# Kernel tuning notes

Measured on AMD Instinct MI355X. Metric: run time of the kernel, lower is better.

The kernel has to match this reference:

```python
import jax, jax.numpy as jnp
import numpy as np

# Instant-NGP hash grid constants (match init_kwargs)
N_MAX, N_MIN = 2048.0, 16.0
L, T, F, DIM = 16, 2**19, 2, 3
NV = 2**DIM  # 8 corners of a voxel
# primes stored as int32 in the original (2654435761 wraps negative) -> replicate exactly
PIS = jnp.asarray(np.array([1, 2654435761, 805459861], dtype=np.uint32).astype(np.int32))
# bin_mask[v, d] = True -> corner v takes floor along dim d
_neigs = np.arange(NV, dtype=np.int64)[:, None]
_dims = np.arange(DIM, dtype=np.int64)[None, :]
BIN_MASK = jnp.asarray((_neigs & (1 << _dims)) == 0)  # [8, 3]
# per-level grid resolutions N_l = N_min * b**l
_b = np.exp((np.log(N_MAX) - np.log(N_MIN)) / L)
SCALES = jnp.asarray((N_MIN * _b ** np.arange(L)).astype(np.float32))  # [L]


def setup_inputs() -> dict:
    key = jax.random.key(0)
    k1, k2 = jax.random.split(key)
    N = 2_000_000
    x = jax.random.uniform(k1, (N, DIM), dtype=jnp.float32)  # points in [0,1)^3 (mu=0, sigma=1)
    # per-level embedding tables, init U(-1e-4, 1e-4) as in the torch module
    W = jax.random.uniform(k2, (L, T, F), minval=-1e-4, maxval=1e-4, dtype=jnp.float32)
    return {"x": x, "W": W}


def _hash(idxs):
    # idxs: [N, 8, 3] int32. int32 wraparound multiply matches low 32 bits of the
    # torch int64 product; since T is a power of two and Python-style mod of a
    # negative by a positive only depends on the low log2(T) bits, result matches.
    prod = idxs * PIS  # [N, 8, 3] int32 (wraps)
    h = prod[..., 0] ^ prod[..., 1] ^ prod[..., 2]
    return h % T  # jnp remainder follows sign of divisor -> nonnegative


def _encode(x, W):
    def level(carry, level_args):
        scale, Wl = level_args
        un_x = x * scale                                   # [N, 3]
        x0 = un_x.astype(jnp.int32)                        # trunc == floor for x >= 0
        diff = jax.lax.stop_gradient(un_x - x0.astype(un_x.dtype))  # [N, 3], detached as in torch
        # corner integer coords: floor where bin_mask else floor+1
        idxs = jnp.where(BIN_MASK[None], x0[:, None, :], x0[:, None, :] + 1)  # [N, 8, 3]
        fv = Wl[_hash(idxs)]                               # [N, 8, F] gather
        wts = jnp.where(BIN_MASK[None], 1.0 - diff[:, None, :], diff[:, None, :])
        wts = wts.prod(axis=-1, keepdims=True)             # [N, 8, 1] trilinear weights
        return carry, (fv * wts).sum(axis=-2)              # [N, F]

    _, ys = jax.lax.scan(level, 0, (SCALES, W))            # [L, N, F]
    # original writes level l into y[:, l*F:(l+1)*F]
    return jnp.transpose(ys, (1, 0, 2)).reshape(x.shape[0], L * F)


def reference(x, W):
    return _encode(x, W)
```

## Files before the change

kernel.cpp:

```cpp
#include <hip/hip_runtime.h>
#include <hip/hip_fp16.h>
#include <math.h>

#define NLEV 16
#define TBLN (1u << 19)
#define TMASK (TBLN - 1u)
#define NPT 4
#define NPTL 16
#define NPTL2 8
#define PR1 2654435761u
#define PR2 805459861u

typedef float f32x4 __attribute__((ext_vector_type(4)));
typedef unsigned int u32;
typedef unsigned int u32x2 __attribute__((ext_vector_type(2)));
typedef unsigned int u32x4 __attribute__((ext_vector_type(4)));

struct ScaleArgs { float s[NLEV]; };

#define DU0 18
#define DU1 23
#define DU2 31
#define GU0 0
#define GU1 5832
#define GU2 17999
#define GUTOT 47790
#define DD2 31
#define DD5 75
#define PO2 0
#define PO5 28830
#define GPTOT2 445080
#define DD3 41
#define DD4 55
#define QO3 0
#define QO4 65600
#define GQTOT 225980

static __device__ __forceinline__ u32 packf2(float a, float b) {
    __half2 h = __floats2half2_rn(a, b);
    return __builtin_bit_cast(u32, h);
}
static __device__ __forceinline__ float2 unpack16(u32 u) {
    __half2 h = __builtin_bit_cast(__half2, u);
    return __half22float2(h);
}
static __device__ __forceinline__ u32 sel4(u32x4 P, u32 idx) {
    u32 s0 = (idx & 1u) ? P.y : P.x;
    u32 s1 = (idx & 1u) ? P.w : P.z;
    return (idx & 2u) ? s1 : s0;
}

__global__ __launch_bounds__(256)
void convert_w(const float* __restrict__ W, u32* __restrict__ Wh, int np4)
{
    int i = blockIdx.x * blockDim.x + threadIdx.x;
    if (i >= np4) return;
    const f32x4* src = reinterpret_cast<const f32x4*>(W) + (size_t)i * 2;
    f32x4 A = __builtin_nontemporal_load(src);
    f32x4 B = __builtin_nontemporal_load(src + 1);
    u32x4 o = { packf2(A.x, A.y), packf2(A.z, A.w),
                packf2(B.x, B.y), packf2(B.z, B.w) };
    __builtin_nontemporal_store(o, reinterpret_cast<u32x4*>(Wh) + i);
}

__global__ __launch_bounds__(256)
void build_unpaired(const float* __restrict__ Wlf, u32* __restrict__ Gu, int D, int P)
{
    int v = blockIdx.x * blockDim.x + threadIdx.x;
    if (v >= P) return;
    int ix = v % D;
    int rest = v / D;
    int iy = rest % D;
    int iz = rest / D;
    u32 h = (((u32)iy * PR1) ^ ((u32)iz * PR2) ^ (u32)ix) & TMASK;
    float2 f = *reinterpret_cast<const float2*>(Wlf + (size_t)h * 2u);
    Gu[v] = packf2(f.x, f.y);
}

__global__ __launch_bounds__(256)
void build_dense(const float* __restrict__ Wlf, u32x2* __restrict__ Gpl, int D, int P)
{
    int v = blockIdx.x * blockDim.x + threadIdx.x;
    if (v >= P) return;
    int Dx = D - 1;
    int ix = v % Dx;
    int rest = v / Dx;
    int iy = rest % D;
    int iz = rest / D;
    u32 e = ((u32)iy * PR1) ^ ((u32)iz * PR2);
    u32 h0 = (e ^ (u32)ix) & TMASK;
    u32 h1 = (e ^ (u32)(ix + 1)) & TMASK;
    float2 f0 = *reinterpret_cast<const float2*>(Wlf + (size_t)h0 * 2u);
    float2 f1 = *reinterpret_cast<const float2*>(Wlf + (size_t)h1 * 2u);
    u32x2 o = { packf2(f0.x, f0.y), packf2(f1.x, f1.y) };
    Gpl[v] = o;
}

__global__ __launch_bounds__(256)
void build_dense16(const float* __restrict__ Wlf, u32x4* __restrict__ Gql, int D, int P)
{
    int v = blockIdx.x * blockDim.x + threadIdx.x;
    if (v >= P) return;
    int Dx = D - 1;
    int ix = v % Dx;
    int rest = v / Dx;
    int iy = rest % Dx;
    int iz = rest / Dx;
    u32 ey0 = ((u32)iy * PR1) ^ ((u32)iz * PR2);
    u32 ey1 = ((u32)(iy + 1) * PR1) ^ ((u32)iz * PR2);
    u32 h00 = (ey0 ^ (u32)ix) & TMASK;
    u32 h10 = (ey0 ^ (u32)(ix + 1)) & TMASK;
    u32 h01 = (ey1 ^ (u32)ix) & TMASK;
    u32 h11 = (ey1 ^ (u32)(ix + 1)) & TMASK;
    float2 f00 = *reinterpret_cast<const float2*>(Wlf + (size_t)h00 * 2u);
    float2 f10 = *reinterpret_cast<const float2*>(Wlf + (size_t)h10 * 2u);
    float2 f01 = *reinterpret_cast<const float2*>(Wlf + (size_t)h01 * 2u);
    float2 f11 = *reinterpret_cast<const float2*>(Wlf + (size_t)h11 * 2u);
    u32x4 o = { packf2(f00.x, f00.y), packf2(f10.x, f10.y),
                packf2(f01.x, f01.y), packf2(f11.x, f11.y) };
    Gql[v] = o;
}

template<int D>
static __device__ __forceinline__ u32 lds_interp(const u32* g, float ux, float uy, float uz)
{
    int ix = (int)ux, iy = (int)uy, iz = (int)uz;
    float dx = ux - (float)ix, dy = uy - (float)iy, dz = uz - (float)iz;
    int b = (iz * D + iy) * D + ix;
    u32 c0 = g[b],             c1 = g[b + 1];
    u32 c2 = g[b + D],         c3 = g[b + D + 1];
    u32 c4 = g[b + D * D],     c5 = g[b + D * D + 1];
    u32 c6 = g[b + D * D + D], c7 = g[b + D * D + D + 1];
    float wxl = 1.f - dx, wxh = dx;
    float wyl = 1.f - dy, wyh = dy;
    float wzl = 1.f - dz, wzh = dz;
    float ax = 0.f, ay = 0.f;
    float2 f;
    f = unpack16(c0); { float w = (wxl * wyl) * wzl; ax = fmaf(f.x, w, ax); ay = fmaf(f.y, w, ay); }
    f = unpack16(c1); { float w = (wxh * wyl) * wzl; ax = fmaf(f.x, w, ax); ay = fmaf(f.y, w, ay); }
    f = unpack16(c2); { float w = (wxl * wyh) * wzl; ax = fmaf(f.x, w, ax); ay = fmaf(f.y, w, ay); }
    f = unpack16(c3); { float w = (wxh * wyh) * wzl; ax = fmaf(f.x, w, ax); ay = fmaf(f.y, w, ay); }
    f = unpack16(c4); { float w = (wxl * wyl) * wzh; ax = fmaf(f.x, w, ax); ay = fmaf(f.y, w, ay); }
    f = unpack16(c5); { float w = (wxh * wyl) * wzh; ax = fmaf(f.x, w, ax); ay = fmaf(f.y, w, ay); }
    f = unpack16(c6); { float w = (wxl * wyh) * wzh; ax = fmaf(f.x, w, ax); ay = fmaf(f.y, w, ay); }
    f = unpack16(c7); { float w = (wxh * wyh) * wzh; ax = fmaf(f.x, w, ax); ay = fmaf(f.y, w, ay); }
    return packf2(ax, ay);
}

template<int D>
__global__ __launch_bounds__(256)
void lds_level(const float* __restrict__ x, const u32* __restrict__ Gu,
               u32* __restrict__ scl, float scale, int N)
{
    __shared__ u32 g[D * D * D];
    for (int i = threadIdx.x; i < D * D * D; i += 256) g[i] = Gu[i];
    __syncthreads();

    int base = blockIdx.x * (256 * NPTL);
    #pragma unroll 4
    for (int i = 0; i < NPTL; ++i) {
        int n = base + i * 256 + (int)threadIdx.x;
        if (n < N) {
            float px = __builtin_nontemporal_load(&x[(size_t)n * 3 + 0]);
            float py = __builtin_nontemporal_load(&x[(size_t)n * 3 + 1]);
            float pz = __builtin_nontemporal_load(&x[(size_t)n * 3 + 2]);
            __builtin_nontemporal_store(
                lds_interp<D>(g, px * scale, py * scale, pz * scale), scl + n);
        }
    }
}

template<int D>
__global__ __launch_bounds__(512)
void lds_level_dyn(const float* __restrict__ x, const u32* __restrict__ Gu,
                   u32* __restrict__ scl, float scale, int N)
{
    extern __shared__ u32 g[];
    for (int i = threadIdx.x; i < D * D * D; i += 512) g[i] = Gu[i];
    __syncthreads();

    int base = blockIdx.x * (512 * NPTL2);
    #pragma unroll 4
    for (int i = 0; i < NPTL2; ++i) {
        int n = base + i * 512 + (int)threadIdx.x;
        if (n < N) {
            float px = __builtin_nontemporal_load(&x[(size_t)n * 3 + 0]);
            float py = __builtin_nontemporal_load(&x[(size_t)n * 3 + 1]);
            float pz = __builtin_nontemporal_load(&x[(size_t)n * 3 + 2]);
            __builtin_nontemporal_store(
                lds_interp<D>(g, px * scale, py * scale, pz * scale), scl + n);
        }
    }
}


template<int D>
static __device__ __forceinline__ void dense_body(
    const float* __restrict__ x, const u32x2* __restrict__ Gp,
    u32* __restrict__ scl, float scale, int N, int TOT, int t)
{
    constexpr int Dx = D - 1;
    constexpr int zstep = D * Dx;

    int nn[NPT];
    float dx[NPT], dy[NPT], dz[NPT];
    int base[NPT];
    u32x2 P0[NPT], P1[NPT], P2[NPT], P3[NPT];

    #pragma unroll
    for (int i = 0; i < NPT; ++i) {
        int n = t + i * TOT;
        if (n > N - 1) n = N - 1;
        nn[i] = n;
        float px = __builtin_nontemporal_load(&x[(size_t)n * 3 + 0]);
        float py = __builtin_nontemporal_load(&x[(size_t)n * 3 + 1]);
        float pz = __builtin_nontemporal_load(&x[(size_t)n * 3 + 2]);
        float ux = px * scale, uy = py * scale, uz = pz * scale;
        int ix = (int)ux, iy = (int)uy, iz = (int)uz;
        dx[i] = ux - (float)ix;
        dy[i] = uy - (float)iy;
        dz[i] = uz - (float)iz;
        base[i] = (iz * D + iy) * Dx + ix;
    }

    #pragma unroll
    for (int i = 0; i < NPT; ++i) {
        int b = base[i];
        P0[i] = Gp[b];
        P1[i] = Gp[b + Dx];
        P2[i] = Gp[b + zstep];
        P3[i] = Gp[b + zstep + Dx];
    }

    #pragma unroll
    for (int i = 0; i < NPT; ++i) {
        float ax = 0.f, ay = 0.f;
        float wxl = 1.f - dx[i], wxh = dx[i];
        float wyl = 1.f - dy[i], wyh = dy[i];
        float wzl = 1.f - dz[i], wzh = dz[i];
        {
            float2 f0 = unpack16(P0[i].x), f1 = unpack16(P0[i].y);
            float w0 = (wxl * wyl) * wzl, w1 = (wxh * wyl) * wzl;
            ax = fmaf(f0.x, w0, ax); ay = fmaf(f0.y, w0, ay);
            ax = fmaf(f1.x, w1, ax); ay = fmaf(f1.y, w1, ay);
        }
        {
            float2 f0 = unpack16(P1[i].x), f1 = unpack16(P1[i].y);
            float w0 = (wxl * wyh) * wzl, w1 = (wxh * wyh) * wzl;
            ax = fmaf(f0.x, w0, ax); ay = fmaf(f0.y, w0, ay);
            ax = fmaf(f1.x, w1, ax); ay = fmaf(f1.y, w1, ay);
        }
        {
            float2 f0 = unpack16(P2[i].x), f1 = unpack16(P2[i].y);
            float w0 = (wxl * wyl) * wzh, w1 = (wxh * wyl) * wzh;
            ax = fmaf(f0.x, w0, ax); ay = fmaf(f0.y, w0, ay);
            ax = fmaf(f1.x, w1, ax); ay = fmaf(f1.y, w1, ay);
        }
        {
            float2 f0 = unpack16(P3[i].x), f1 = unpack16(P3[i].y);
            float w0 = (wxl * wyh) * wzh, w1 = (wxh * wyh) * wzh;
            ax = fmaf(f0.x, w0, ax); ay = fmaf(f0.y, w0, ay);
            ax = fmaf(f1.x, w1, ax); ay = fmaf(f1.y, w1, ay);
        }
        __builtin_nontemporal_store(packf2(ax, ay), scl + nn[i]);
    }
}

template<int D>
static __device__ __forceinline__ void dense16_body(
    const float* __restrict__ x, const u32x4* __restrict__ Gq,
    u32* __restrict__ scl, float scale, int N, int TOT, int t)
{
    constexpr int Dx = D - 1;
    constexpr int zstep = Dx * Dx;

    int nn[NPT];
    float dx[NPT], dy[NPT], dz[NPT];
    int base[NPT];
    u32x4 Q0[NPT], Q1[NPT];

    #pragma unroll
    for (int i = 0; i < NPT; ++i) {
        int n = t + i * TOT;
        if (n > N - 1) n = N - 1;
        nn[i] = n;
        float px = __builtin_nontemporal_load(&x[(size_t)n * 3 + 0]);
        float py = __builtin_nontemporal_load(&x[(size_t)n * 3 + 1]);
        float pz = __builtin_nontemporal_load(&x[(size_t)n * 3 + 2]);
        float ux = px * scale, uy = py * scale, uz = pz * scale;
        int ix = (int)ux, iy = (int)uy, iz = (int)uz;
        dx[i] = ux - (float)ix;
        dy[i] = uy - (float)iy;
        dz[i] = uz - (float)iz;
        base[i] = (iz * Dx + iy) * Dx + ix;
    }

    #pragma unroll
    for (int i = 0; i < NPT; ++i) {
        Q0[i] = Gq[base[i]];
        Q1[i] = Gq[base[i] + zstep];
    }

    #pragma unroll
    for (int i = 0; i < NPT; ++i) {
        float ax = 0.f, ay = 0.f;
        float wxl = 1.f - dx[i], wxh = dx[i];
        float wyl = 1.f - dy[i], wyh = dy[i];
        float wzl = 1.f - dz[i], wzh = dz[i];
        float2 f;
        f = unpack16(Q0[i].x); { float w = (wxl * wyl) * wzl; ax = fmaf(f.x, w, ax); ay = fmaf(f.y, w, ay); }
        f = unpack16(Q0[i].y); { float w = (wxh * wyl) * wzl; ax = fmaf(f.x, w, ax); ay = fmaf(f.y, w, ay); }
        f = unpack16(Q0[i].z); { float w = (wxl * wyh) * wzl; ax = fmaf(f.x, w, ax); ay = fmaf(f.y, w, ay); }
        f = unpack16(Q0[i].w); { float w = (wxh * wyh) * wzl; ax = fmaf(f.x, w, ax); ay = fmaf(f.y, w, ay); }
        f = unpack16(Q1[i].x); { float w = (wxl * wyl) * wzh; ax = fmaf(f.x, w, ax); ay = fmaf(f.y, w, ay); }
        f = unpack16(Q1[i].y); { float w = (wxh * wyl) * wzh; ax = fmaf(f.x, w, ax); ay = fmaf(f.y, w, ay); }
        f = unpack16(Q1[i].z); { float w = (wxl * wyh) * wzh; ax = fmaf(f.x, w, ax); ay = fmaf(f.y, w, ay); }
        f = unpack16(Q1[i].w); { float w = (wxh * wyh) * wzh; ax = fmaf(f.x, w, ax); ay = fmaf(f.y, w, ay); }
        __builtin_nontemporal_store(packf2(ax, ay), scl + nn[i]);
    }
}

static __device__ __forceinline__ void hash_body(
    const float* __restrict__ x, const u32* __restrict__ Wl,
    u32* __restrict__ scl, float scale, int N, int TOT, int t)
{
    int nn[NPT];
    float dx[NPT], dy[NPT], dz[NPT];
    u32 a0[NPT], a1[NPT], a2[NPT];
    u32 fv[NPT][8];

    #pragma unroll
    for (int i = 0; i < NPT; ++i) {
        int n = t + i * TOT;
        if (n > N - 1) n = N - 1;
        nn[i] = n;
        float px = __builtin_nontemporal_load(&x[(size_t)n * 3 + 0]);
        float py = __builtin_nontemporal_load(&x[(size_t)n * 3 + 1]);
        float pz = __builtin_nontemporal_load(&x[(size_t)n * 3 + 2]);
        float ux = px * scale, uy = py * scale, uz = pz * scale;
        int ix = (int)ux, iy = (int)uy, iz = (int)uz;
        dx[i] = ux - (float)ix;
        dy[i] = uy - (float)iy;
        dz[i] = uz - (float)iz;
        a0[i] = (unsigned)ix;
        a1[i] = (unsigned)iy * PR1;
        a2[i] = (unsigned)iz * PR2;
    }

    #pragma unroll
    for (int i = 0; i < NPT; ++i) {
        u32 b0 = a0[i] + 1u, b1 = a1[i] + PR1, b2 = a2[i] + PR2;
        u32 E[4] = { a1[i] ^ a2[i], b1 ^ a2[i], a1[i] ^ b2, b1 ^ b2 };
        u32 par = a0[i] & 3u;
        if ((par & 1u) == 0u) {
            #pragma unroll
            for (int j = 0; j < 4; ++j) {
                u32 hl = (E[j] ^ a0[i]) & TMASK;
                u32x2 p = *reinterpret_cast<const u32x2*>(Wl + (hl & ~1u));
                fv[i][2 * j + 0] = (hl & 1u) ? p.y : p.x;
                fv[i][2 * j + 1] = (hl & 1u) ? p.x : p.y;
            }
        } else if (par == 1u) {
            #pragma unroll
            for (int j = 0; j < 4; ++j) {
                u32 hl = (E[j] ^ a0[i]) & TMASK;
                u32x4 P = *reinterpret_cast<const u32x4*>(Wl + (hl & ~3u));
                u32 il = hl & 3u;
                fv[i][2 * j + 0] = sel4(P, il);
                fv[i][2 * j + 1] = sel4(P, il ^ 3u);
            }
        } else {
            #pragma unroll
            for (int j = 0; j < 4; ++j) {
                u32 hl = (E[j] ^ a0[i]) & TMASK;
                u32 hh = (E[j] ^ b0) & TMASK;
                fv[i][2 * j + 0] = Wl[hl];
                fv[i][2 * j + 1] = Wl[hh];
            }
        }
    }

    #pragma unroll
    for (int i = 0; i < NPT; ++i) {
        float ax = 0.f, ay = 0.f;
        #pragma unroll
        for (int v = 0; v < 8; ++v) {
            float wx = (v & 1) ? dx[i] : 1.f - dx[i];
            float wy = (v & 2) ? dy[i] : 1.f - dy[i];
            float wz = (v & 4) ? dz[i] : 1.f - dz[i];
            float w = (wx * wy) * wz;
            float2 f = unpack16(fv[i][v]);
            ax = fmaf(f.x, w, ax);
            ay = fmaf(f.y, w, ay);
        }
        __builtin_nontemporal_store(packf2(ax, ay), scl + nn[i]);
    }
}

__global__ __launch_bounds__(256)
void fused_levels(const float* __restrict__ x, const u32* __restrict__ Wh,
                  const u32x2* __restrict__ Gp, const u32x4* __restrict__ Gq,
                  u32* __restrict__ scratch,
                  ScaleArgs sc, int N, int TOT, int BPL, int lstart)
{
    int li = blockIdx.x / BPL;
    int lvl = li + lstart;
    int t = (blockIdx.x - li * BPL) * blockDim.x + threadIdx.x;
    if (t >= TOT) return;
    float scale = sc.s[lvl];
    u32* scl = scratch + (size_t)lvl * (size_t)N;

    switch (lvl) {
        case 2: dense_body<DD2>(x, Gp + PO2, scl, scale, N, TOT, t); break;
        case 3: dense16_body<DD3>(x, Gq + QO3, scl, scale, N, TOT, t); break;
        case 4: dense16_body<DD4>(x, Gq + QO4, scl, scale, N, TOT, t); break;
        case 5: dense_body<DD5>(x, Gp + PO5, scl, scale, N, TOT, t); break;
        default:
            hash_body(x, Wh + (size_t)(lvl - 6) * TBLN, scl, scale, N, TOT, t);
            break;
    }
}

__global__ __launch_bounds__(256)
void transpose_kernel(const u32* __restrict__ sc, float* __restrict__ out, int N)
{
    __shared__ u32 lds[16][257];
    int P0 = blockIdx.x * 256;
    int t = threadIdx.x;
    #pragma unroll
    for (int l = 0; l < NLEV; ++l) {
        int n = P0 + t;
        if (n < N) lds[l][t] = __builtin_nontemporal_load(sc + (size_t)l * N + n);
    }
    __syncthreads();
    int w = t >> 6, l6 = t & 63;
    #pragma unroll
    for (int k = 0; k < 8; ++k) {
        int p = w * 64 + k * 8 + (l6 >> 3);
        int c = l6 & 7;
        if (P0 + p < N) {
            float2 f0 = unpack16(lds[2 * c][p]);
            float2 f1 = unpack16(lds[2 * c + 1][p]);
            f32x4 v = { f0.x, f0.y, f1.x, f1.y };
            __builtin_nontemporal_store(v,
                reinterpret_cast<f32x4*>(out + (size_t)(P0 + p) * 32u + (size_t)c * 4u));
        }
    }
}

__global__ __launch_bounds__(256)
void hashenc_fallback(const float* __restrict__ x, const float* __restrict__ W,
                      float* __restrict__ out, ScaleArgs sc, int N)
{
    int n = blockIdx.x * blockDim.x + threadIdx.x;
    if (n >= N) return;
    float px = x[(size_t)n * 3 + 0];
    float py = x[(size_t)n * 3 + 1];
    float pz = x[(size_t)n * 3 + 2];
    float acc[2 * NLEV];
    #pragma unroll
    for (int l = 0; l < NLEV; ++l) {
        float s = sc.s[l];
        float ux = px * s, uy = py * s, uz = pz * s;
        int ix = (int)ux, iy = (int)uy, iz = (int)uz;
        float dx = ux - (float)ix, dy = uy - (float)iy, dz = uz - (float)iz;
        unsigned a0 = (unsigned)ix;
        unsigned a1 = (unsigned)iy * PR1;
        unsigned a2 = (unsigned)iz * PR2;
        unsigned b0 = a0 + 1u, b1 = a1 + PR1, b2 = a2 + PR2;
        const float* Wl = W + (size_t)l * TBLN * 2u;
        float ax = 0.f, ay = 0.f;
        #pragma unroll
        for (int v = 0; v < 8; ++v) {
            unsigned h = ((v & 1) ? b0 : a0) ^ ((v & 2) ? b1 : a1) ^ ((v & 4) ? b2 : a2);
            h &= TMASK;
            float wx = (v & 1) ? dx : 1.f - dx;
            float wy = (v & 2) ? dy : 1.f - dy;
            float wz = (v & 4) ? dz : 1.f - dz;
            float w = (wx * wy) * wz;
            const float2 fvv = *reinterpret_cast<const float2*>(Wl + (size_t)h * 2u);
            ax = fmaf(fvv.x, w, ax);
            ay = fmaf(fvv.y, w, ay);
        }
        acc[2 * l + 0] = ax;
        acc[2 * l + 1] = ay;
    }
    float4* o = reinterpret_cast<float4*>(out + (size_t)n * (2 * NLEV));
    #pragma unroll
    for (int j = 0; j < 8; ++j)
        o[j] = make_float4(acc[4 * j + 0], acc[4 * j + 1], acc[4 * j + 2], acc[4 * j + 3]);
}

extern "C" void kernel_launch(void* const* d_in, const int* in_sizes, int n_in,
                              void* d_out, int out_size, void* d_ws, size_t ws_size,
                              hipStream_t stream) {
    const float* x = (const float*)d_in[0];
    const float* W = (const float*)d_in[1];
    float* out = (float*)d_out;
    int N = in_sizes[0] / 3;

    ScaleArgs sc;
    double b = exp((log(2048.0) - log(16.0)) / 16.0);
    for (int l = 0; l < NLEV; ++l) {
        double p;
        switch (l) {
            case 0: p = 1.0; break;
            case 1: p = b;   break;
            case 2: p = b * b; break;
            default: p = pow(b, (double)l); break;
        }
        sc.s[l] = (float)(16.0 * p);
    }

    size_t wh_u32 = (size_t)(NLEV - 6) * TBLN;
    size_t gp_u32 = (size_t)GPTOT2 * 2u;
    size_t gq_u32 = (size_t)GQTOT * 4u;
    size_t gu_u32 = (size_t)GUTOT;
    size_t scr_u32 = (size_t)NLEV * (size_t)N;
    size_t need = (wh_u32 + gp_u32 + gq_u32 + gu_u32 + scr_u32) * sizeof(u32);

    if (ws_size >= need) {
        u32* Wh = (u32*)d_ws;
        u32x2* Gp = reinterpret_cast<u32x2*>(Wh + wh_u32);
        u32x4* Gq = reinterpret_cast<u32x4*>(Wh + wh_u32 + gp_u32);
        u32* Gu = Wh + wh_u32 + gp_u32 + gq_u32;
        u32* scratch = Gu + gu_u32;

        size_t l2_lds_bytes = (size_t)DU2 * DU2 * DU2 * sizeof(u32);
        bool lvl2_lds = (hipFuncSetAttribute(
                             (const void*)&lds_level_dyn<DU2>,
                             hipFuncAttributeMaxDynamicSharedMemorySize,
                             (int)l2_lds_bytes) == hipSuccess);

        int np4 = (int)(wh_u32 / 4);
        hipLaunchKernelGGL(convert_w, dim3((np4 + 255) / 256), dim3(256), 0, stream,
                           W + (size_t)6 * TBLN * 2u, Wh, np4);

        {
            int P0c = DU0 * DU0 * DU0;
            hipLaunchKernelGGL(build_unpaired, dim3((P0c + 255) / 256), dim3(256), 0, stream,
                               W + 0, Gu + GU0, DU0, P0c);
            int P1c = DU1 * DU1 * DU1;
            hipLaunchKernelGGL(build_unpaired, dim3((P1c + 255) / 256), dim3(256), 0, stream,
                               W + (size_t)1 * TBLN * 2u, Gu + GU1, DU1, P1c);
            int P2c = DU2 * DU2 * DU2;
            hipLaunchKernelGGL(build_unpaired, dim3((P2c + 255) / 256), dim3(256), 0, stream,
                               W + (size_t)2 * TBLN * 2u, Gu + GU2, DU2, P2c);
        }

        {
            int P2 = (DD2 - 1) * DD2 * DD2;
            hipLaunchKernelGGL(build_dense, dim3((P2 + 255) / 256), dim3(256), 0, stream,
                               W + (size_t)2 * TBLN * 2u, Gp + PO2, DD2, P2);
            int P5 = (DD5 - 1) * DD5 * DD5;
            hipLaunchKernelGGL(build_dense, dim3((P5 + 255) / 256), dim3(256), 0, stream,
                               W + (size_t)5 * TBLN * 2u, Gp + PO5, DD5, P5);
        }

        {
            int P3 = DD3 * (DD3 - 1) * (DD3 - 1);
            hipLaunchKernelGGL(build_dense16, dim3((P3 + 255) / 256), dim3(256), 0, stream,
                               W + (size_t)3 * TBLN * 2u, Gq + QO3, DD3, P3);
            int P4 = DD4 * (DD4 - 1) * (DD4 - 1);
            hipLaunchKernelGGL(build_dense16, dim3((P4 + 255) / 256), dim3(256), 0, stream,
                               W + (size_t)4 * TBLN * 2u, Gq + QO4, DD4, P4);
        }

        {
            int blocks = (N + 256 * NPTL - 1) / (256 * NPTL);
            hipLaunchKernelGGL(lds_level<DU0>, dim3(blocks), dim3(256), 0, stream,
                               x, Gu + GU0, scratch + 0, sc.s[0], N);
            hipLaunchKernelGGL(lds_level<DU1>, dim3(blocks), dim3(256), 0, stream,
                               x, Gu + GU1, scratch + (size_t)N, sc.s[1], N);
        }

        if (lvl2_lds) {
            int blocks = (N + 512 * NPTL2 - 1) / (512 * NPTL2);
            hipLaunchKernelGGL(lds_level_dyn<DU2>, dim3(blocks), dim3(512),
                               l2_lds_bytes, stream,
                               x, Gu + GU2, scratch + (size_t)2 * N, sc.s[2], N);
        }

        int lstart = lvl2_lds ? 3 : 2;
        int TOT = (N + NPT - 1) / NPT;
        int BPL = (TOT + 255) / 256;
        hipLaunchKernelGGL(fused_levels, dim3((16 - lstart) * BPL), dim3(256), 0, stream,
                           x, Wh, Gp, Gq, scratch, sc, N, TOT, BPL, lstart);

        int gt = (N + 255) / 256;
        hipLaunchKernelGGL(transpose_kernel, dim3(gt), dim3(256), 0, stream,
                           scratch, out, N);
    } else {
        int grid = (N + 255) / 256;
        hipLaunchKernelGGL(hashenc_fallback, dim3(grid), dim3(256), 0, stream,
                           x, W, out, sc, N);
    }
}
```

Baseline: 607.0 us.

## Merge table-build kernels into one launch and fuse LDS levels 0 and 1

Replaces the eight separate preprocessing launches (fp16 weight conversion plus the unpaired, dense and dense16 grid builds) with a single build_all kernel that dispatches on global thread index ranges. It also fuses the level 0 and level 1 LDS interpolation kernels into one 512-thread kernel that holds both grids in shared memory and reads each point once. The aim is to cut launch overhead and tail idle time, and to halve reads of x for these two levels. The cost is branch divergence at range boundaries and a larger LDS footprint per block, which may lower occupancy.

```diff
diff --git a/kernel.cpp b/kernel.cpp
--- a/kernel.cpp
+++ b/kernel.cpp
@@ -35,6 +35,15 @@
 #define QO3 0
 #define QO4 65600
 #define GQTOT 225980
+#define NP4 1310720
+#define B1 1310720
+#define B2 1316552
+#define B3 1328719
+#define B4 1358510
+#define B5 1387340
+#define B6 1803590
+#define B7 1869190
+#define BT 2029570
 
 static __device__ __forceinline__ u32 packf2(float a, float b) {
     __half2 h = __floats2half2_rn(a, b);
@@ -50,11 +59,9 @@
     return (idx & 2u) ? s1 : s0;
 }
 
-__global__ __launch_bounds__(256)
-void convert_w(const float* __restrict__ W, u32* __restrict__ Wh, int np4)
-{
-    int i = blockIdx.x * blockDim.x + threadIdx.x;
-    if (i >= np4) return;
+static __device__ __forceinline__ void conv_item(const float* __restrict__ W,
+                                                 u32* __restrict__ Wh, int i)
+{
     const f32x4* src = reinterpret_cast<const f32x4*>(W) + (size_t)i * 2;
     f32x4 A = __builtin_nontemporal_load(src);
     f32x4 B = __builtin_nontemporal_load(src + 1);
@@ -62,12 +69,9 @@
                 packf2(B.x, B.y), packf2(B.z, B.w) };
     __builtin_nontemporal_store(o, reinterpret_cast<u32x4*>(Wh) + i);
 }
-
-__global__ __launch_bounds__(256)
-void build_unpaired(const float* __restrict__ Wlf, u32* __restrict__ Gu, int D, int P)
-{
-    int v = blockIdx.x * blockDim.x + threadIdx.x;
-    if (v >= P) return;
+static __device__ __forceinline__ void unp_item(const float* __restrict__ Wlf,
+                                                u32* __restrict__ Gu, int D, int v)
+{
     int ix = v % D;
     int rest = v / D;
     int iy = rest % D;
@@ -76,12 +80,9 @@
     float2 f = *reinterpret_cast<const float2*>(Wlf + (size_t)h * 2u);
     Gu[v] = packf2(f.x, f.y);
 }
-
-__global__ __launch_bounds__(256)
-void build_dense(const float* __restrict__ Wlf, u32x2* __restrict__ Gpl, int D, int P)
-{
-    int v = blockIdx.x * blockDim.x + threadIdx.x;
-    if (v >= P) return;
+static __device__ __forceinline__ void dens_item(const float* __restrict__ Wlf,
+                                                 u32x2* __restrict__ Gpl, int D, int v)
+{
     int Dx = D - 1;
     int ix = v % Dx;
     int rest = v / Dx;
@@ -95,12 +96,9 @@
     u32x2 o = { packf2(f0.x, f0.y), packf2(f1.x, f1.y) };
     Gpl[v] = o;
 }
-
-__global__ __launch_bounds__(256)
-void build_dense16(const float* __restrict__ Wlf, u32x4* __restrict__ Gql, int D, int P)
-{
-    int v = blockIdx.x * blockDim.x + threadIdx.x;
-    if (v >= P) return;
+static __device__ __forceinline__ void dens16_item(const float* __restrict__ Wlf,
+                                                   u32x4* __restrict__ Gql, int D, int v)
+{
     int Dx = D - 1;
     int ix = v % Dx;
     int rest = v / Dx;
@@ -119,6 +117,21 @@
     u32x4 o = { packf2(f00.x, f00.y), packf2(f10.x, f10.y),
                 packf2(f01.x, f01.y), packf2(f11.x, f11.y) };
     Gql[v] = o;
+}
+
+__global__ __launch_bounds__(256)
+void build_all(const float* __restrict__ W, u32* __restrict__ Wh,
+               u32* __restrict__ Gu, u32x2* __restrict__ Gp, u32x4* __restrict__ Gq)
+{
+    int g = blockIdx.x * blockDim.x + threadIdx.x;
+    if (g < B1)      conv_item(W + (size_t)6 * TBLN * 2u, Wh, g);
+    else if (g < B2) unp_item(W, Gu + GU0, DU0, g - B1);
+    else if (g < B3) unp_item(W + (size_t)1 * TBLN * 2u, Gu + GU1, DU1, g - B2);
+    else if (g < B4) unp_item(W + (size_t)2 * TBLN * 2u, Gu + GU2, DU2, g - B3);
+    else if (g < B5) dens_item(W + (size_t)2 * TBLN * 2u, Gp + PO2, DD2, g - B4);
+    else if (g < B6) dens_item(W + (size_t)5 * TBLN * 2u, Gp + PO5, DD5, g - B5);
+    else if (g < B7) dens16_item(W + (size_t)3 * TBLN * 2u, Gq + QO3, DD3, g - B6);
+    else if (g < BT) dens16_item(W + (size_t)4 * TBLN * 2u, Gq + QO4, DD4, g - B7);
 }
 
 template<int D>
@@ -145,6 +158,33 @@
     f = unpack16(c6); { float w = (wxl * wyh) * wzh; ax = fmaf(f.x, w, ax); ay = fmaf(f.y, w, ay); }
     f = unpack16(c7); { float w = (wxh * wyh) * wzh; ax = fmaf(f.x, w, ax); ay = fmaf(f.y, w, ay); }
     return packf2(ax, ay);
+}
+
+__global__ __launch_bounds__(512)
+void lds_level01(const float* __restrict__ x, const u32* __restrict__ Gu,
+                 u32* __restrict__ scratch, float s0, float s1, int N)
+{
+    extern __shared__ u32 g[];
+    u32* g0 = g;
+    u32* g1 = g + DU0 * DU0 * DU0;
+    for (int i = threadIdx.x; i < DU0 * DU0 * DU0; i += 512) g0[i] = Gu[GU0 + i];
+    for (int i = threadIdx.x; i < DU1 * DU1 * DU1; i += 512) g1[i] = Gu[GU1 + i];
+    __syncthreads();
+
+    int base = blockIdx.x * (512 * NPTL);
+    #pragma unroll 4
+    for (int i = 0; i < NPTL; ++i) {
+        int n = base + i * 512 + (int)threadIdx.x;
+        if (n < N) {
+            float px = __builtin_nontemporal_load(&x[(size_t)n * 3 + 0]);
+            float py = __builtin_nontemporal_load(&x[(size_t)n * 3 + 1]);
+            float pz = __builtin_nontemporal_load(&x[(size_t)n * 3 + 2]);
+            __builtin_nontemporal_store(
+                lds_interp<DU0>(g0, px * s0, py * s0, pz * s0), scratch + n);
+            __builtin_nontemporal_store(
+                lds_interp<DU1>(g1, px * s1, py * s1, pz * s1), scratch + (size_t)N + n);
+        }
+    }
 }
 
 template<int D>
@@ -526,47 +566,26 @@
         u32* Gu = Wh + wh_u32 + gp_u32 + gq_u32;
         u32* scratch = Gu + gu_u32;
 
+        size_t l01_lds_bytes = (size_t)(DU0 * DU0 * DU0 + DU1 * DU1 * DU1) * sizeof(u32);
+        bool lvl01_lds = (hipFuncSetAttribute(
+                              (const void*)&lds_level01,
+                              hipFuncAttributeMaxDynamicSharedMemorySize,
+                              (int)l01_lds_bytes) == hipSuccess);
         size_t l2_lds_bytes = (size_t)DU2 * DU2 * DU2 * sizeof(u32);
         bool lvl2_lds = (hipFuncSetAttribute(
                              (const void*)&lds_level_dyn<DU2>,
                              hipFuncAttributeMaxDynamicSharedMemorySize,
                              (int)l2_lds_bytes) == hipSuccess);
 
-        int np4 = (int)(wh_u32 / 4);
-        hipLaunchKernelGGL(convert_w, dim3((np4 + 255) / 256), dim3(256), 0, stream,
-                           W + (size_t)6 * TBLN * 2u, Wh, np4);
-
-        {
-            int P0c = DU0 * DU0 * DU0;
-            hipLaunchKernelGGL(build_unpaired, dim3((P0c + 255) / 256), dim3(256), 0, stream,
-                               W + 0, Gu + GU0, DU0, P0c);
-            int P1c = DU1 * DU1 * DU1;
-            hipLaunchKernelGGL(build_unpaired, dim3((P1c + 255) / 256), dim3(256), 0, stream,
-                               W + (size_t)1 * TBLN * 2u, Gu + GU1, DU1, P1c);
-            int P2c = DU2 * DU2 * DU2;
-            hipLaunchKernelGGL(build_unpaired, dim3((P2c + 255) / 256), dim3(256), 0, stream,
-                               W + (size_t)2 * TBLN * 2u, Gu + GU2, DU2, P2c);
-        }
-
-        {
-            int P2 = (DD2 - 1) * DD2 * DD2;
-            hipLaunchKernelGGL(build_dense, dim3((P2 + 255) / 256), dim3(256), 0, stream,
-                               W + (size_t)2 * TBLN * 2u, Gp + PO2, DD2, P2);
-            int P5 = (DD5 - 1) * DD5 * DD5;
-            hipLaunchKernelGGL(build_dense, dim3((P5 + 255) / 256), dim3(256), 0, stream,
-                               W + (size_t)5 * TBLN * 2u, Gp + PO5, DD5, P5);
-        }
-
-        {
-            int P3 = DD3 * (DD3 - 1) * (DD3 - 1);
-            hipLaunchKernelGGL(build_dense16, dim3((P3 + 255) / 256), dim3(256), 0, stream,
-                               W + (size_t)3 * TBLN * 2u, Gq + QO3, DD3, P3);
-            int P4 = DD4 * (DD4 - 1) * (DD4 - 1);
-            hipLaunchKernelGGL(build_dense16, dim3((P4 + 255) / 256), dim3(256), 0, stream,
-                               W + (size_t)4 * TBLN * 2u, Gq + QO4, DD4, P4);
-        }
-
-        {
+        hipLaunchKernelGGL(build_all, dim3((BT + 255) / 256), dim3(256), 0, stream,
+                           W, Wh, Gu, Gp, Gq);
+
+        if (lvl01_lds) {
+            int blocks = (N + 512 * NPTL - 1) / (512 * NPTL);
+            hipLaunchKernelGGL(lds_level01, dim3(blocks), dim3(512),
+                               l01_lds_bytes, stream,
+                               x, Gu, scratch, sc.s[0], sc.s[1], N);
+        } else {
             int blocks = (N + 256 * NPTL - 1) / (256 * NPTL);
             hipLaunchKernelGGL(lds_level<DU0>, dim3(blocks), dim3(256), 0, stream,
                                x, Gu + GU0, scratch + 0, sc.s[0], N);
```

Result: faster. 581.9 us (-4.1%).
